# Kernel optimization log

Measured on AMD Instinct MI355X. Metric: run time of the kernel, lower is better.

Reference implementation:

```python
import jax, jax.numpy as jnp
import numpy as np

N_EMBD = 384
HEAD_SIZE = 16

def setup_inputs() -> dict:
    key = jax.random.key(0)
    k1, k2, k3, k4 = jax.random.split(key, 4)
    B, T = 4, 4096
    x = jax.random.normal(k1, (B, T, N_EMBD), dtype=jnp.float32)
    # nn.Linear(n_embd, head_size, bias=False): y = x @ W^T, W: [head_size, n_embd].
    # Store transposed [n_embd, head_size] for direct matmul.
    s = 1.0 / np.sqrt(N_EMBD)
    Wk = jax.random.uniform(k2, (N_EMBD, HEAD_SIZE), jnp.float32, -s, s)
    Wq = jax.random.uniform(k3, (N_EMBD, HEAD_SIZE), jnp.float32, -s, s)
    Wv = jax.random.uniform(k4, (N_EMBD, HEAD_SIZE), jnp.float32, -s, s)
    return {"x": x, "Wk": Wk, "Wq": Wq, "Wv": Wv}

def reference(x, Wk, Wq, Wv):
    B, T, C = x.shape
    k = x @ Wk  # [B,T,H]
    q = x @ Wq
    v = x @ Wv
    scale = k.shape[-1] ** -0.5
    wei = jnp.einsum('bth,bsh->bts', q, k) * scale  # [B,T,T]
    causal = jnp.tril(jnp.ones((T, T), dtype=bool))
    wei = jnp.where(causal, wei, -jnp.inf)
    wei = jax.nn.softmax(wei, axis=-1)
    out = jnp.einsum('bts,bsh->bth', wei, v)  # [B,T,H]
    return out
```

## Files before the change

### kernel.cpp

```cpp
#include <hip/hip_runtime.h>


constexpr int B_DIM = 4;
constexpr int T_SEQ = 4096;
constexpr int C_DIM = 384;
constexpr int H_DIM = 16;
constexpr int NROW  = B_DIM * T_SEQ;
constexpr int NSLOT = 16;

typedef __bf16 bf16x8 __attribute__((ext_vector_type(8)));
typedef float  f32x4  __attribute__((ext_vector_type(4)));

__device__ __forceinline__ unsigned short f2bf(float f) {
  unsigned int u = __builtin_bit_cast(unsigned int, f);
  u += 0x7fffu + ((u >> 16) & 1u);
  return (unsigned short)(u >> 16);
}
__device__ __forceinline__ bf16x8 as_bf16x8(uint4 u) {
  return __builtin_bit_cast(bf16x8, u);
}
__device__ __forceinline__ unsigned cvt_pk_bf16(float lo, float hi) {
  unsigned r;
  asm("v_cvt_pk_bf16_f32 %0, %1, %2" : "=v"(r) : "v"(lo), "v"(hi));
  return r;
}

__global__ __launch_bounds__(256) void wconv(
    const float* __restrict__ Wk, const float* __restrict__ Wq,
    const float* __restrict__ Wv, unsigned short* __restrict__ WT) {
  const int i = blockIdx.x * 256 + threadIdx.x;
  const int m = i / 6144;
  const int r = i - m * 6144;
  const int n = r / 384;
  const int k = r - n * 384;
  const float* __restrict__ W = (m == 0) ? Wk : (m == 1) ? Wq : Wv;
  WT[i] = f2bf(W[k * 16 + n]);
}

__global__ __launch_bounds__(128) void qkv_mfma(
    const float* __restrict__ x, const unsigned short* __restrict__ WT,
    unsigned short* __restrict__ Kb,
    unsigned short* __restrict__ Qb,
    unsigned short* __restrict__ VTb)
{
  const int tid  = threadIdx.x;
  const int w    = tid >> 6;
  const int lane = tid & 63;
  const int quad = lane >> 4;
  const int col  = lane & 15;
  const int r0   = blockIdx.x << 4;
  const int kb   = w * 6;

  __shared__ float mrg[12][64];

  const float4* __restrict__ xp =
      reinterpret_cast<const float4*>(x + (size_t)(r0 + col) * C_DIM) + quad * 2;
  float4 araw[12];
#pragma unroll
  for (int kk = 0; kk < 6; ++kk) {
    araw[2 * kk]     = xp[(kb + kk) * 8];
    araw[2 * kk + 1] = xp[(kb + kk) * 8 + 1];
  }

  const uint4* __restrict__ bk = reinterpret_cast<const uint4*>(
      WT + (size_t)col * 384 + quad * 8);
  const uint4* __restrict__ bq = bk + 768;
  const uint4* __restrict__ bv = bk + 1536;

  f32x4 ck = {0.f, 0.f, 0.f, 0.f};
  f32x4 cq = {0.f, 0.f, 0.f, 0.f};
  f32x4 cv = {0.f, 0.f, 0.f, 0.f};
#pragma unroll
  for (int kk = 0; kk < 6; ++kk) {
    uint4 pk;
    const float4 a0 = araw[2 * kk], a1 = araw[2 * kk + 1];
    pk.x = cvt_pk_bf16(a0.x, a0.y);
    pk.y = cvt_pk_bf16(a0.z, a0.w);
    pk.z = cvt_pk_bf16(a1.x, a1.y);
    pk.w = cvt_pk_bf16(a1.z, a1.w);
    const bf16x8 av = as_bf16x8(pk);
    ck = __builtin_amdgcn_mfma_f32_16x16x32_bf16(av, as_bf16x8(bk[(kb + kk) * 4]), ck, 0, 0, 0);
    cq = __builtin_amdgcn_mfma_f32_16x16x32_bf16(av, as_bf16x8(bq[(kb + kk) * 4]), cq, 0, 0, 0);
    cv = __builtin_amdgcn_mfma_f32_16x16x32_bf16(av, as_bf16x8(bv[(kb + kk) * 4]), cv, 0, 0, 0);
  }

  if (w == 1) {
#pragma unroll
    for (int r = 0; r < 4; ++r) {
      mrg[r][lane]     = ck[r];
      mrg[4 + r][lane] = cq[r];
      mrg[8 + r][lane] = cv[r];
    }
  }
  __syncthreads();
  if (w == 0) {
    const float SC = 0.25f * 1.44269504088896341f;
#pragma unroll
    for (int r = 0; r < 4; ++r) {
      const float vk = ck[r] + mrg[r][lane];
      const float vq = cq[r] + mrg[4 + r][lane];
      const float vv = cv[r] + mrg[8 + r][lane];
      const int row = r0 + quad * 4 + r;
      Kb[row * 16 + col]      = f2bf(vk);
      Qb[row * 32 + col]      = f2bf(vq * SC);
      Qb[row * 32 + 16 + col] = 0;
      const int bb = row >> 12, t = row & 4095;
      VTb[(((size_t)(bb * 16 + col)) << 12) + t] = f2bf(vv);
    }
  }
}

__global__ __launch_bounds__(256) void flash_v8(
    const unsigned short* __restrict__ Qb,
    const unsigned short* __restrict__ Kb,
    const unsigned short* __restrict__ VTb,
    float* __restrict__ PO, float* __restrict__ PL)
{
  const int tid  = threadIdx.x;
  const int w    = tid >> 6;
  const int lane = tid & 63;
  const int quad = lane >> 4;
  const int col  = lane & 15;
  const int p    = blockIdx.x >> 4;
  const int b    = (blockIdx.x >> 2) & 3;
  const int j    = blockIdx.x & 3;
  const int slot = (j << 2) | w;
  const int qtA  = 255 - p;
  const int qtB  = p;
  const int nchA = (qtA + 4) >> 2;

  __shared__ __attribute__((aligned(16))) unsigned short Pl[4][16 * 72];
  unsigned short* const P = Pl[w];

  const unsigned short* Kbase = Kb + ((size_t)(b * T_SEQ) << 4);
  const unsigned short* Vbase = VTb + (((size_t)(b * 16 + col)) << 12);
  const int poff = col * 72 + quad * 4;

  f32x4 o = {0.f, 0.f, 0.f, 0.f};

  const uint4* qpA = reinterpret_cast<const uint4*>(
      Qb + (((size_t)(b * T_SEQ + (qtA << 4) + col)) << 5) + quad * 8);
  const uint4* qpB = reinterpret_cast<const uint4*>(
      Qb + (((size_t)(b * T_SEQ + (qtB << 4) + col)) << 5) + quad * 8);
  const bf16x8 qaA = as_bf16x8(qpA[0]);
  const bf16x8 qaB = as_bf16x8(qpB[0]);

  auto loadK = [&](int c, uint4* k4) {
    const int kt0 = c << 2;
#pragma unroll
    for (int t = 0; t < 4; ++t)
      k4[t] = *reinterpret_cast<const uint4*>(
          Kbase + (((size_t)((kt0 + t) * 16 + col)) << 4) + quad * 8);
  };
  auto loadV = [&](int c, uint4* v2) {
    v2[0] = *reinterpret_cast<const uint4*>(Vbase + c * 64 + quad * 8);
    v2[1] = *reinterpret_cast<const uint4*>(Vbase + c * 64 + 32 + quad * 8);
  };

  auto computeP = [&](int qt, bf16x8 qa, int c, const uint4* k4, float& lref) {
    const int kt0 = c << 2;
    float lsum = 0.f;
#pragma unroll
    for (int t = 0; t < 4; ++t) {
      const int kt = kt0 + t;
      f32x4 sf;
      if (kt <= qt) {
        f32x4 z = {0.f, 0.f, 0.f, 0.f};
        sf = __builtin_amdgcn_mfma_f32_16x16x32_bf16(as_bf16x8(k4[t]), qa, z, 0, 0, 0);
        if (kt == qt) {
#pragma unroll
          for (int r = 0; r < 4; ++r)
            if (quad * 4 + r > col) sf[r] = -1e30f;
        }
      } else {
#pragma unroll
        for (int r = 0; r < 4; ++r) sf[r] = -1e30f;
      }
      const float p0 = __builtin_amdgcn_exp2f(sf[0]);
      const float p1 = __builtin_amdgcn_exp2f(sf[1]);
      const float p2 = __builtin_amdgcn_exp2f(sf[2]);
      const float p3 = __builtin_amdgcn_exp2f(sf[3]);
      lsum += (p0 + p1) + (p2 + p3);
      uint2 pr;
      pr.x = cvt_pk_bf16(p0, p1);
      pr.y = cvt_pk_bf16(p2, p3);
      *reinterpret_cast<uint2*>(P + poff + t * 16) = pr;
    }
    lref += lsum;
  };

  auto doPV = [&](const uint4* v2) {
    const uint2* pp = reinterpret_cast<const uint2*>(P + col * 72);
    const uint2 a0 = pp[quad * 2],     a1 = pp[quad * 2 + 1];
    const uint2 b0 = pp[8 + quad * 2], b1 = pp[8 + quad * 2 + 1];
    const uint4 p0 = {a0.x, a0.y, a1.x, a1.y};
    const uint4 p1 = {b0.x, b0.y, b1.x, b1.y};
    o = __builtin_amdgcn_mfma_f32_16x16x32_bf16(as_bf16x8(p0), as_bf16x8(v2[0]), o, 0, 0, 0);
    o = __builtin_amdgcn_mfma_f32_16x16x32_bf16(as_bf16x8(p1), as_bf16x8(v2[1]), o, 0, 0, 0);
  };

  auto writePartial = [&](int qt, float lsum) {
    float l = lsum;
    l += __shfl_xor(l, 16);
    l += __shfl_xor(l, 32);
    const size_t rowbase = (size_t)b * T_SEQ + ((size_t)qt << 4);
    float* pO = PO + ((size_t)slot * NROW + rowbase) * 16;
#pragma unroll
    for (int r = 0; r < 4; ++r)
      pO[(quad * 4 + r) * 16 + col] = o[r];
    if (quad == 0) PL[(size_t)slot * NROW + rowbase + col] = l;
  };

  float lA = 0.f, lB = 0.f;
  uint4 k4[4], vcur[2], vnxt[2];

  int g = slot;
  loadK(g, k4);
  loadV(g, vcur);
  computeP(qtA, qaA, g, k4, lA);

  int prevg = g;
  g += 16;
  while (g < 65) {
    const int c = (g < nchA) ? g : g - nchA;
    loadK(c, k4);
    loadV(c, vnxt);
    doPV(vcur);
    asm volatile("" ::: "memory");
    if (prevg < nchA && g >= nchA) {
      writePartial(qtA, lA);
      o = (f32x4){0.f, 0.f, 0.f, 0.f};
    }
    if (g < nchA) computeP(qtA, qaA, c, k4, lA);
    else          computeP(qtB, qaB, c, k4, lB);
    vcur[0] = vnxt[0];
    vcur[1] = vnxt[1];
    prevg = g;
    g += 16;
  }
  doPV(vcur);
  if (prevg < nchA) {
    writePartial(qtA, lA);
    o = (f32x4){0.f, 0.f, 0.f, 0.f};
    writePartial(qtB, 0.f);
  } else {
    writePartial(qtB, lB);
  }
}

__global__ __launch_bounds__(256) void flash_merge(
    const float* __restrict__ PO, const float* __restrict__ PL,
    float* __restrict__ out)
{
  const int i   = blockIdx.x * 256 + threadIdx.x;
  const int row = i >> 4;
  float O = 0.f, L = 0.f;
#pragma unroll
  for (int s = 0; s < NSLOT; ++s) {
    O += PO[((size_t)s * NROW) * 16 + i];
    L += PL[(size_t)s * NROW + row];
  }
  out[i] = O / L;
}

extern "C" void kernel_launch(void* const* d_in, const int* in_sizes, int n_in,
                              void* d_out, int out_size, void* d_ws, size_t ws_size,
                              hipStream_t stream) {
  const float* x  = (const float*)d_in[0];
  const float* Wk = (const float*)d_in[1];
  const float* Wq = (const float*)d_in[2];
  const float* Wv = (const float*)d_in[3];
  float* outp = (float*)d_out;

  unsigned short* Qb  = (unsigned short*)d_ws;
  unsigned short* Kb  = Qb + (size_t)NROW * 32;
  unsigned short* VTb = Kb + (size_t)NROW * 16 + 64;
  unsigned short* WT  = VTb + (size_t)NROW * 16;
  float* PO = (float*)(WT + 18432);
  float* PL = PO + (size_t)NSLOT * NROW * 16;

  wconv<<<72, 256, 0, stream>>>(Wk, Wq, Wv, WT);
  qkv_mfma<<<1024, 128, 0, stream>>>(x, WT, Kb, Qb, VTb);
  flash_v8<<<2048, 256, 0, stream>>>(Qb, Kb, VTb, PO, PL);
  flash_merge<<<1024, 256, 0, stream>>>(PO, PL, outp);
}
```

Before: 102.7 us.

## Fuse split-K merge into attention kernel via shared-memory reduction across 8 waves

The flash kernel now runs 512 blocks of 8 waves each, and all the key chunks for a query-tile pair are processed inside one block instead of being spread over 4 blocks. Partial outputs and row sums are written to shared memory and reduced in-block after a barrier, then normalized and stored directly. This removes the separate merge kernel, its launch, and the global round-trip of 16 partial slots. The cost is fewer blocks (512 vs 2048), a larger block with more shared memory, and an end-of-kernel barrier that may reduce occupancy and load balance.

```diff
diff --git a/kernel.cpp b/kernel.cpp
--- a/kernel.cpp
+++ b/kernel.cpp
@@ -6,7 +6,6 @@
 constexpr int C_DIM = 384;
 constexpr int H_DIM = 16;
 constexpr int NROW  = B_DIM * T_SEQ;
-constexpr int NSLOT = 16;
 
 typedef __bf16 bf16x8 __attribute__((ext_vector_type(8)));
 typedef float  f32x4  __attribute__((ext_vector_type(4)));
@@ -110,26 +109,26 @@
   }
 }
 
-__global__ __launch_bounds__(256) void flash_v8(
+__global__ __launch_bounds__(512) void flash_v9(
     const unsigned short* __restrict__ Qb,
     const unsigned short* __restrict__ Kb,
     const unsigned short* __restrict__ VTb,
-    float* __restrict__ PO, float* __restrict__ PL)
+    float* __restrict__ out)
 {
   const int tid  = threadIdx.x;
   const int w    = tid >> 6;
   const int lane = tid & 63;
   const int quad = lane >> 4;
   const int col  = lane & 15;
-  const int p    = blockIdx.x >> 4;
-  const int b    = (blockIdx.x >> 2) & 3;
-  const int j    = blockIdx.x & 3;
-  const int slot = (j << 2) | w;
+  const int p    = blockIdx.x >> 2;
+  const int b    = blockIdx.x & 3;
   const int qtA  = 255 - p;
   const int qtB  = p;
   const int nchA = (qtA + 4) >> 2;
 
-  __shared__ __attribute__((aligned(16))) unsigned short Pl[4][16 * 72];
+  __shared__ __attribute__((aligned(16))) unsigned short Pl[8][16 * 72];
+  __shared__ float mO[8][2][256];
+  __shared__ float mL[8][2][16];
   unsigned short* const P = Pl[w];
 
   const unsigned short* Kbase = Kb + ((size_t)(b * T_SEQ) << 4);
@@ -199,28 +198,26 @@
     o = __builtin_amdgcn_mfma_f32_16x16x32_bf16(as_bf16x8(p1), as_bf16x8(v2[1]), o, 0, 0, 0);
   };
 
-  auto writePartial = [&](int qt, float lsum) {
+  auto writePartial = [&](int ph, float lsum) {
     float l = lsum;
     l += __shfl_xor(l, 16);
     l += __shfl_xor(l, 32);
-    const size_t rowbase = (size_t)b * T_SEQ + ((size_t)qt << 4);
-    float* pO = PO + ((size_t)slot * NROW + rowbase) * 16;
 #pragma unroll
     for (int r = 0; r < 4; ++r)
-      pO[(quad * 4 + r) * 16 + col] = o[r];
-    if (quad == 0) PL[(size_t)slot * NROW + rowbase + col] = l;
+      mO[w][ph][(quad * 4 + r) * 16 + col] = o[r];
+    if (quad == 0) mL[w][ph][col] = l;
   };
 
   float lA = 0.f, lB = 0.f;
   uint4 k4[4], vcur[2], vnxt[2];
 
-  int g = slot;
+  int g = w;
   loadK(g, k4);
   loadV(g, vcur);
   computeP(qtA, qaA, g, k4, lA);
 
   int prevg = g;
-  g += 16;
+  g += 8;
   while (g < 65) {
     const int c = (g < nchA) ? g : g - nchA;
     loadK(c, k4);
@@ -228,7 +225,7 @@
     doPV(vcur);
     asm volatile("" ::: "memory");
     if (prevg < nchA && g >= nchA) {
-      writePartial(qtA, lA);
+      writePartial(0, lA);
       o = (f32x4){0.f, 0.f, 0.f, 0.f};
     }
     if (g < nchA) computeP(qtA, qaA, c, k4, lA);
@@ -236,31 +233,31 @@
     vcur[0] = vnxt[0];
     vcur[1] = vnxt[1];
     prevg = g;
-    g += 16;
+    g += 8;
   }
   doPV(vcur);
   if (prevg < nchA) {
-    writePartial(qtA, lA);
+    writePartial(0, lA);
     o = (f32x4){0.f, 0.f, 0.f, 0.f};
-    writePartial(qtB, 0.f);
+    writePartial(1, 0.f);
   } else {
-    writePartial(qtB, lB);
-  }
-}
-
-__global__ __launch_bounds__(256) void flash_merge(
-    const float* __restrict__ PO, const float* __restrict__ PL,
-    float* __restrict__ out)
-{
-  const int i   = blockIdx.x * 256 + threadIdx.x;
-  const int row = i >> 4;
-  float O = 0.f, L = 0.f;
-#pragma unroll
-  for (int s = 0; s < NSLOT; ++s) {
-    O += PO[((size_t)s * NROW) * 16 + i];
-    L += PL[(size_t)s * NROW + row];
-  }
-  out[i] = O / L;
+    writePartial(1, lB);
+  }
+
+  __syncthreads();
+
+  {
+    const int ph = tid >> 8;
+    const int i  = tid & 255;
+    float O = 0.f, L = 0.f;
+#pragma unroll
+    for (int ww = 0; ww < 8; ++ww) {
+      O += mO[ww][ph][i];
+      L += mL[ww][ph][i >> 4];
+    }
+    const int qt = ph ? qtB : qtA;
+    out[(size_t)(b * T_SEQ + (qt << 4)) * 16 + i] = O / L;
+  }
 }
 
 extern "C" void kernel_launch(void* const* d_in, const int* in_sizes, int n_in,
@@ -276,11 +273,8 @@
   unsigned short* Kb  = Qb + (size_t)NROW * 32;
   unsigned short* VTb = Kb + (size_t)NROW * 16 + 64;
   unsigned short* WT  = VTb + (size_t)NROW * 16;
-  float* PO = (float*)(WT + 18432);
-  float* PL = PO + (size_t)NSLOT * NROW * 16;
 
   wconv<<<72, 256, 0, stream>>>(Wk, Wq, Wv, WT);
   qkv_mfma<<<1024, 128, 0, stream>>>(x, WT, Kb, Qb, VTb);
-  flash_v8<<<2048, 256, 0, stream>>>(Qb, Kb, VTb, PO, PL);
-  flash_merge<<<1024, 256, 0, stream>>>(PO, PL, outp);
-}
+  flash_v9<<<512, 512, 0, stream>>>(Qb, Kb, VTb, outp);
+}
```

Result: faster. 94.82 us (-7.7%).
